# Kernel optimization log

Measured on AMD Instinct MI355X. Metric: run time of the kernel, lower is better.

## Reference

```python
import jax, jax.numpy as jnp
import numpy as np

RSQRT2 = 2 ** (-0.5)
B, S, D_IN = 2, 4096, 1024
H, D_HEAD = 8, 64            # num_heads, attention_dim (per-head qk and v dim)
QK_DIM = H * D_HEAD          # 512
V_DIM = H * D_HEAD           # 512
OUT_DIM = D_IN               # 1024 (output_dim defaults to input_dim)
LN_EPS = 1e-5


def setup_inputs() -> dict:
    key = jax.random.key(0)
    ks = jax.random.split(key, 8)
    def lecun(k, fan_in, shape):
        return jax.random.normal(k, shape, dtype=jnp.float32) * (1.0 / np.sqrt(fan_in))
    return {
        "x": jax.random.normal(ks[0], (B, S, D_IN), dtype=jnp.float32),
        # weights stored [in, out] (transposed torch Linear layout)
        "W_qk": lecun(ks[1], D_IN, (D_IN, 2 * QK_DIM)),
        "b_qk": jnp.zeros((2 * QK_DIM,), jnp.float32),
        "W_v": lecun(ks[2], D_IN, (D_IN, V_DIM)),
        "b_v": jnp.zeros((V_DIM,), jnp.float32),
        "W_out": lecun(ks[3], V_DIM, (V_DIM, OUT_DIM)),
        "b_out": jnp.zeros((OUT_DIM,), jnp.float32),
        "ln_gamma": jnp.ones((OUT_DIM,), jnp.float32),
        "ln_beta": jnp.zeros((OUT_DIM,), jnp.float32),
    }


def _layernorm(y, gamma, beta):
    mu = jnp.mean(y, axis=-1, keepdims=True)
    var = jnp.mean(jnp.square(y - mu), axis=-1, keepdims=True)
    return (y - mu) * jax.lax.rsqrt(var + LN_EPS) * gamma + beta


def reference(x, W_qk, b_qk, W_v, b_v, W_out, b_out, ln_gamma, ln_beta):
    b, s, _ = x.shape
    scale = D_HEAD ** (-0.5)
    qk = x @ W_qk + b_qk                          # [b, s, 2*h*d]
    qk = qk.reshape(b, s, H, D_HEAD, 2)           # c (q/k) is fastest axis
    q, k = qk[..., 0], qk[..., 1]                 # [b, s, h, d]
    v = (x @ W_v + b_v).reshape(b, s, H, D_HEAD)  # [b, s, h, d]
    # manual multi-head attention, full O(s^2) score matrix (as in source)
    sim = jnp.einsum("bihd,bjhd->bhij", q, k) * scale
    attn = jax.nn.softmax(sim, axis=-1)           # [b, h, i, j]
    o = jnp.einsum("bhij,bjhd->bihd", attn, v)    # [b, s, h, d]
    o = o.reshape(b, s, V_DIM)                    # 'b h s d -> b s (h d)'
    y = _layernorm(o @ W_out + b_out, ln_gamma, ln_beta)
    return (y + x) * RSQRT2
```

## Files before the change

kernel.cpp:

```cpp
#include <hip/hip_runtime.h>
#include <stdint.h>

typedef short bf16x8 __attribute__((ext_vector_type(8)));
typedef float f32x4 __attribute__((ext_vector_type(4)));
typedef unsigned short ushort_t;

#define RSQRT2_F 0.70710678118654752440f
#define QSCALE_F 0.18033688011114382f

__device__ __forceinline__ ushort_t f2bf(float f) {
  union { float f; uint32_t u; } c; c.f = f;
  uint32_t u = c.u;
  uint32_t r = (u + 0x7fffu + ((u >> 16) & 1u)) >> 16;
  return (ushort_t)r;
}
__device__ __forceinline__ float bf2f(ushort_t u) {
  union { uint32_t u; float f; } c; c.u = ((uint32_t)u) << 16;
  return c.f;
}
__device__ __forceinline__ uint32_t fbits(float f) {
  union { float f; uint32_t u; } c; c.f = f; return c.u;
}

__device__ __forceinline__ void gload_lds16(const void* g, void* l) {
  __builtin_amdgcn_global_load_lds(
      (const __attribute__((address_space(1))) void*)g,
      (__attribute__((address_space(3))) void*)l, 16, 0, 0);
}

__global__ __launch_bounds__(256) void k_cvt_x(const float* __restrict__ x,
                                               ushort_t* __restrict__ xb) {
  int i = (blockIdx.x * 256 + threadIdx.x) * 4;
  float4 f = *(const float4*)(x + i);
  ushort4 o;
  o.x = f2bf(f.x); o.y = f2bf(f.y); o.z = f2bf(f.z); o.w = f2bf(f.w);
  *(ushort4*)(xb + i) = o;
}

__global__ __launch_bounds__(256) void k_build_wqkv(const float* __restrict__ Wqk,
                                                    const float* __restrict__ bqk,
                                                    const float* __restrict__ Wv,
                                                    const float* __restrict__ bv,
                                                    ushort_t* __restrict__ Wt,
                                                    float* __restrict__ biasAll) {
  int k = blockIdx.x * 256 + threadIdx.x;
  int n = blockIdx.y;
  float w, bb;
  if (n < 512)       { w = Wqk[(size_t)k * 1024 + 2 * n] * QSCALE_F;     bb = bqk[2 * n] * QSCALE_F; }
  else if (n < 1024) { w = Wqk[(size_t)k * 1024 + 2 * (n - 512) + 1];    bb = bqk[2 * (n - 512) + 1]; }
  else               { w = Wv[(size_t)k * 512 + (n - 1024)];             bb = bv[n - 1024]; }
  Wt[(size_t)n * 1024 + k] = f2bf(w);
  if (k == 0) biasAll[n] = bb;
}

__global__ __launch_bounds__(256) void k_build_wout(const float* __restrict__ Wout,
                                                    ushort_t* __restrict__ Wt) {
  int k = blockIdx.x * 256 + threadIdx.x;
  int n = blockIdx.y;
  Wt[(size_t)n * 512 + k] = f2bf(Wout[(size_t)k * 1024 + n]);
}

template <int MODE>
__global__ __launch_bounds__(256) void k_gemm_bt(
    const ushort_t* __restrict__ A, const ushort_t* __restrict__ Bt,
    const float* __restrict__ bias,
    ushort_t* __restrict__ out0, ushort_t* __restrict__ out1, ushort_t* __restrict__ out2,
    int M, int N, int K) {
  __shared__ __align__(16) ushort_t As[2][4][128][8];
  __shared__ __align__(16) ushort_t Bs[2][4][128][8];
  const int t = threadIdx.x;
  const int lane = t & 63;
  const int wave = t >> 6;

  const int nby = N >> 7;
  const int nwg = gridDim.x;
  const int xcd = blockIdx.x & 7, pos = blockIdx.x >> 3;
  const int swz = xcd * (nwg >> 3) + pos;
  const int bx = swz / nby, by = swz % nby;
  const int m0 = bx * 128, n0 = by * 128;

  const int wm = (wave >> 1) * 64, wn = (wave & 1) * 64;
  const int lg = lane >> 4, lr = lane & 15;

  const int srow = t & 127, sg = t >> 7;
  const ushort_t* gA = A + (size_t)(m0 + srow) * K + sg * 8;
  const ushort_t* gB = Bt + (size_t)(n0 + srow) * K + sg * 8;

  f32x4 acc[4][4] = {};

#define GEMM_STAGE(k0, bsel)                                   \
  do {                                                         \
    gload_lds16(gA + (k0), &As[bsel][sg][srow][0]);            \
    gload_lds16(gA + (k0) + 16, &As[bsel][sg + 2][srow][0]);   \
    gload_lds16(gB + (k0), &Bs[bsel][sg][srow][0]);            \
    gload_lds16(gB + (k0) + 16, &Bs[bsel][sg + 2][srow][0]);   \
  } while (0)

  GEMM_STAGE(0, 0);
  __syncthreads();
  int buf = 0;
  for (int k0 = 0; k0 < K; k0 += 32) {
    if (k0 + 32 < K) GEMM_STAGE(k0 + 32, buf ^ 1);
    bf16x8 af[4], bfr[4];
#pragma unroll
    for (int mi = 0; mi < 4; mi++) af[mi] = *(const bf16x8*)&As[buf][lg][wm + mi * 16 + lr][0];
#pragma unroll
    for (int ni = 0; ni < 4; ni++) bfr[ni] = *(const bf16x8*)&Bs[buf][lg][wn + ni * 16 + lr][0];
#pragma unroll
    for (int mi = 0; mi < 4; mi++)
#pragma unroll
      for (int ni = 0; ni < 4; ni++)
        acc[mi][ni] = __builtin_amdgcn_mfma_f32_16x16x32_bf16(af[mi], bfr[ni], acc[mi][ni], 0, 0, 0);
    __syncthreads();
    buf ^= 1;
  }
#undef GEMM_STAGE

#pragma unroll
  for (int mi = 0; mi < 4; mi++) {
    int rowb = m0 + wm + mi * 16 + (lane >> 4) * 4;
#pragma unroll
    for (int ni = 0; ni < 4; ni++) {
      int col = n0 + wn + ni * 16 + lr;
      float bc = bias[col];
#pragma unroll
      for (int reg = 0; reg < 4; reg++) {
        int row = rowb + reg;
        float v = acc[mi][ni][reg] + bc;
        if (MODE == 0) {
          if (col < 512) {
            out0[(size_t)row * 512 + col] = f2bf(v);
          } else if (col < 1024) {
            out1[(size_t)row * 512 + (col - 512)] = f2bf(v);
          } else {
            int hd = col - 1024;
            int bb = row >> 12, s = row & 4095;
            out2[((size_t)(bb << 9) + hd) * 4096 + s] = f2bf(v);
          }
        } else {
          out0[(size_t)row * 1024 + col] = f2bf(v);
        }
      }
    }
  }
}

__global__ __launch_bounds__(256, 2) void k_attn(const ushort_t* __restrict__ Qb,
                                                 const ushort_t* __restrict__ Kb,
                                                 const ushort_t* __restrict__ Vt,
                                                 ushort_t* __restrict__ O0,
                                                 ushort_t* __restrict__ O1,
                                                 ushort_t* __restrict__ O2,
                                                 ushort_t* __restrict__ O3,
                                                 float* __restrict__ lpart) {
  __shared__ __align__(16) ushort_t Ks[2][8][64][8];
  __shared__ __align__(16) ushort_t Vs[2][8][64][8];
  __shared__ __align__(16) ushort_t Pl[4][1024];
  const int S = 4096;
  const int t = threadIdx.x, lane = t & 63, wave = t >> 6;
  const int lg = lane >> 4, lr = lane & 15;

  const int bid = blockIdx.x;
  const int xcd = bid & 7, idx = bid >> 3;
  const int bh = (xcd << 1) | (idx >> 6);
  const int rem = idx & 63;
  const int qb = rem >> 2;
  const int quarter = rem & 3;
  const int b = bh >> 3, h = bh & 7;
  const int qbase = qb * 256 + wave * 64;
  const int kvbase = quarter * 1024;

  bf16x8 qf[4][2];
#pragma unroll
  for (int su = 0; su < 4; su++) {
    const ushort_t* qp = Qb + ((size_t)(b * S + qbase + su * 16 + lr)) * 512 + h * 64 + lg * 8;
    qf[su][0] = *(const bf16x8*)qp;
    qf[su][1] = *(const bf16x8*)(qp + 32);
  }

  const int cj = t & 63, cg = t >> 6;
  const ushort_t* gK = Kb + ((size_t)b * S + cj) * 512 + h * 64 + cg * 8;
  const ushort_t* gV = Vt + ((size_t)bh * 64 + cj) * 4096 + cg * 8;

  const bf16x8 vones = {(short)0x3F80, (short)0x3F80, (short)0x3F80, (short)0x3F80,
                        (short)0x3F80, (short)0x3F80, (short)0x3F80, (short)0x3F80};

  int poff[4], pread[2];
#pragma unroll
  for (int nt = 0; nt < 4; nt++) poff[nt] = (lr * 128 + nt * 32 + lg * 8) ^ ((lr & 7) << 4);
#pragma unroll
  for (int kc = 0; kc < 2; kc++) pread[kc] = (lr * 128 + kc * 64 + lg * 16) ^ ((lr & 7) << 4);

  f32x4 of[4][4] = {};
  f32x4 of_sum[4] = {};

#define ATTN_STAGE(kv0, bsel)                                         \
  do {                                                                \
    gload_lds16(gK + (size_t)(kv0) * 512, &Ks[bsel][cg][cj][0]);      \
    gload_lds16(gK + (size_t)(kv0) * 512 + 32, &Ks[bsel][cg + 4][cj][0]); \
    gload_lds16(gV + (kv0), &Vs[bsel][cg][cj][0]);                    \
    gload_lds16(gV + (kv0) + 32, &Vs[bsel][cg + 4][cj][0]);           \
  } while (0)

  ATTN_STAGE(kvbase, 0);
  __syncthreads();
  int buf = 0;

  for (int kv0 = kvbase; kv0 < kvbase + 1024; kv0 += 64) {
    if (kv0 + 64 < kvbase + 1024) ATTN_STAGE(kv0 + 64, buf ^ 1);

    f32x4 sf[4][4];
    __builtin_amdgcn_s_setprio(1);
#pragma unroll
    for (int nt = 0; nt < 4; nt++) {
      bf16x8 kf0 = *(const bf16x8*)&Ks[buf][lg][nt * 16 + lr][0];
      bf16x8 kf1 = *(const bf16x8*)&Ks[buf][4 + lg][nt * 16 + lr][0];
#pragma unroll
      for (int su = 0; su < 4; su++) {
        f32x4 z = {};
        z = __builtin_amdgcn_mfma_f32_16x16x32_bf16(kf0, qf[su][0], z, 0, 0, 0);
        sf[su][nt] = __builtin_amdgcn_mfma_f32_16x16x32_bf16(kf1, qf[su][1], z, 0, 0, 0);
      }
    }
    __builtin_amdgcn_s_setprio(0);

    bf16x8 pf[4][2];
#pragma unroll
    for (int su = 0; su < 4; su++) {
      char* Pb = (char*)&Pl[wave][0];
#pragma unroll
      for (int nt = 0; nt < 4; nt++) {
        float p0 = __builtin_amdgcn_exp2f(sf[su][nt][0]);
        float p1 = __builtin_amdgcn_exp2f(sf[su][nt][1]);
        float p2 = __builtin_amdgcn_exp2f(sf[su][nt][2]);
        float p3 = __builtin_amdgcn_exp2f(sf[su][nt][3]);
        uint32_t w0 = (fbits(p0) >> 16) | (fbits(p1) & 0xffff0000u);
        uint32_t w1 = (fbits(p2) >> 16) | (fbits(p3) & 0xffff0000u);
        *(uint2*)(Pb + poff[nt]) = make_uint2(w0, w1);
      }
#pragma unroll
      for (int kc = 0; kc < 2; kc++) pf[su][kc] = *(const bf16x8*)(Pb + pread[kc]);
    }

    __builtin_amdgcn_s_setprio(1);
#pragma unroll
    for (int dt = 0; dt < 4; dt++) {
      bf16x8 vf0 = *(const bf16x8*)&Vs[buf][lg][dt * 16 + lr][0];
      bf16x8 vf1 = *(const bf16x8*)&Vs[buf][4 + lg][dt * 16 + lr][0];
#pragma unroll
      for (int su = 0; su < 4; su++) {
        of[su][dt] = __builtin_amdgcn_mfma_f32_16x16x32_bf16(pf[su][0], vf0, of[su][dt], 0, 0, 0);
        of[su][dt] = __builtin_amdgcn_mfma_f32_16x16x32_bf16(pf[su][1], vf1, of[su][dt], 0, 0, 0);
      }
    }
#pragma unroll
    for (int su = 0; su < 4; su++) {
      of_sum[su] = __builtin_amdgcn_mfma_f32_16x16x32_bf16(pf[su][0], vones, of_sum[su], 0, 0, 0);
      of_sum[su] = __builtin_amdgcn_mfma_f32_16x16x32_bf16(pf[su][1], vones, of_sum[su], 0, 0, 0);
    }
    __builtin_amdgcn_s_setprio(0);

    __syncthreads();
    buf ^= 1;
  }
#undef ATTN_STAGE

  ushort_t* Opq = (quarter == 0) ? O0 : (quarter == 1) ? O1 : (quarter == 2) ? O2 : O3;
  ushort_t* Opw = Opq + (size_t)b * 4096 * 512;
#pragma unroll
  for (int su = 0; su < 4; su++) {
#pragma unroll
    for (int dt = 0; dt < 4; dt++)
#pragma unroll
      for (int r = 0; r < 4; r++) {
        int q = qbase + su * 16 + lg * 4 + r;
        Opw[(size_t)q * 512 + h * 64 + dt * 16 + lr] = f2bf(of[su][dt][r]);
      }
    if (lr == 0) {
#pragma unroll
      for (int r = 0; r < 4; r++) {
        int q = qbase + su * 16 + lg * 4 + r;
        lpart[(((size_t)quarter * 2 + b) * 8 + h) * 4096 + q] = of_sum[su][r];
      }
    }
  }
}

__global__ __launch_bounds__(128) void k_merge(const ushort_t* __restrict__ O0,
                                               const ushort_t* __restrict__ O1,
                                               const ushort_t* __restrict__ O2,
                                               const ushort_t* __restrict__ O3,
                                               const float* __restrict__ lpart,
                                               ushort_t* __restrict__ Ob) {
  const int row = blockIdx.x;
  const int t = threadIdx.x;
  const int col = t * 4;
  const int b = row >> 12, q = row & 4095;
  const int h = col >> 6;
  float l = 0.f;
#pragma unroll
  for (int qu = 0; qu < 4; qu++)
    l += lpart[(((size_t)qu * 2 + b) * 8 + h) * 4096 + q];
  float inv = 1.0f / l;
  ushort4 a0 = *(const ushort4*)(O0 + (size_t)row * 512 + col);
  ushort4 a1 = *(const ushort4*)(O1 + (size_t)row * 512 + col);
  ushort4 a2 = *(const ushort4*)(O2 + (size_t)row * 512 + col);
  ushort4 a3 = *(const ushort4*)(O3 + (size_t)row * 512 + col);
  ushort4 o;
  o.x = f2bf((bf2f(a0.x) + bf2f(a1.x) + bf2f(a2.x) + bf2f(a3.x)) * inv);
  o.y = f2bf((bf2f(a0.y) + bf2f(a1.y) + bf2f(a2.y) + bf2f(a3.y)) * inv);
  o.z = f2bf((bf2f(a0.z) + bf2f(a1.z) + bf2f(a2.z) + bf2f(a3.z)) * inv);
  o.w = f2bf((bf2f(a0.w) + bf2f(a1.w) + bf2f(a2.w) + bf2f(a3.w)) * inv);
  *(ushort4*)(Ob + (size_t)row * 512 + col) = o;
}

__global__ __launch_bounds__(256) void k_ln(const ushort_t* __restrict__ ypre,
                                            const float* __restrict__ x,
                                            const float* __restrict__ gamma,
                                            const float* __restrict__ beta,
                                            float* __restrict__ out) {
  __shared__ float red[8];
  const int row = blockIdx.x, t = threadIdx.x;
  const ushort_t* yr = ypre + (size_t)row * 1024;
  ushort4 u = *(const ushort4*)(yr + t * 4);
  float v0 = bf2f(u.x), v1 = bf2f(u.y), v2 = bf2f(u.z), v3 = bf2f(u.w);
  float s = v0 + v1 + v2 + v3;
  float sq = v0 * v0 + v1 * v1 + v2 * v2 + v3 * v3;
#pragma unroll
  for (int m = 32; m; m >>= 1) { s += __shfl_xor(s, m, 64); sq += __shfl_xor(sq, m, 64); }
  if ((t & 63) == 0) { red[t >> 6] = s; red[4 + (t >> 6)] = sq; }
  __syncthreads();
  s = red[0] + red[1] + red[2] + red[3];
  sq = red[4] + red[5] + red[6] + red[7];
  float mu = s * (1.f / 1024.f);
  float var = sq * (1.f / 1024.f) - mu * mu;
  float inv = rsqrtf(var + 1e-5f);
  int c = t * 4;
  float4 xf = *(const float4*)(x + (size_t)row * 1024 + c);
  float4 o;
  o.x = ((v0 - mu) * inv * gamma[c + 0] + beta[c + 0] + xf.x) * RSQRT2_F;
  o.y = ((v1 - mu) * inv * gamma[c + 1] + beta[c + 1] + xf.y) * RSQRT2_F;
  o.z = ((v2 - mu) * inv * gamma[c + 2] + beta[c + 2] + xf.z) * RSQRT2_F;
  o.w = ((v3 - mu) * inv * gamma[c + 3] + beta[c + 3] + xf.w) * RSQRT2_F;
  *(float4*)(out + (size_t)row * 1024 + c) = o;
}

extern "C" void kernel_launch(void* const* d_in, const int* in_sizes, int n_in,
                              void* d_out, int out_size, void* d_ws, size_t ws_size,
                              hipStream_t stream) {
  (void)in_sizes; (void)n_in; (void)out_size; (void)ws_size;
  const float* x     = (const float*)d_in[0];
  const float* Wqk   = (const float*)d_in[1];
  const float* bqk   = (const float*)d_in[2];
  const float* Wv    = (const float*)d_in[3];
  const float* bv    = (const float*)d_in[4];
  const float* Wout  = (const float*)d_in[5];
  const float* bout  = (const float*)d_in[6];
  const float* gamma = (const float*)d_in[7];
  const float* beta  = (const float*)d_in[8];
  float* out = (float*)d_out;

  char* ws = (char*)d_ws;
  size_t off = 0;
  auto alloc = [&](size_t bytes) {
    off = (off + 255) & ~(size_t)255;
    void* p = ws + off;
    off += bytes;
    return p;
  };
  ushort_t* xb    = (ushort_t*)alloc(8192ull * 1024 * 2);
  ushort_t* Wqkvt = (ushort_t*)alloc(1536ull * 1024 * 2);
  float*    biasA = (float*)   alloc(1536ull * 4);
  ushort_t* Woutt = (ushort_t*)alloc(1024ull * 512 * 2);
  ushort_t* Qb    = (ushort_t*)alloc(8192ull * 512 * 2);
  ushort_t* Kbuf  = (ushort_t*)alloc(8192ull * 512 * 2);
  ushort_t* Vtb   = (ushort_t*)alloc(1024ull * 4096 * 2);
  ushort_t* Oq2   = (ushort_t*)alloc(8192ull * 512 * 2);
  ushort_t* Oq3   = (ushort_t*)alloc(8192ull * 512 * 2);
  float*    lpart = (float*)   alloc(4ull * 2 * 8 * 4096 * 4);
  ushort_t* Oq0   = xb;
  ushort_t* Oq1   = xb + 8192ull * 512;
  ushort_t* Obm   = Qb;
  ushort_t* ypre  = xb;

  k_cvt_x<<<8192, 256, 0, stream>>>(x, xb);
  k_build_wqkv<<<dim3(4, 1536), 256, 0, stream>>>(Wqk, bqk, Wv, bv, Wqkvt, biasA);
  k_build_wout<<<dim3(2, 1024), 256, 0, stream>>>(Wout, Woutt);
  k_gemm_bt<0><<<768, 256, 0, stream>>>(xb, Wqkvt, biasA, Qb, Kbuf, Vtb, 8192, 1536, 1024);
  k_attn<<<1024, 256, 0, stream>>>(Qb, Kbuf, Vtb, Oq0, Oq1, Oq2, Oq3, lpart);
  k_merge<<<8192, 128, 0, stream>>>(Oq0, Oq1, Oq2, Oq3, lpart, Obm);
  k_gemm_bt<1><<<512, 256, 0, stream>>>(Obm, Woutt, bout, ypre, nullptr, nullptr, 8192, 1024, 512);
  k_ln<<<8192, 256, 0, stream>>>(ypre, x, gamma, beta, out);
}
```

Baseline: 207.4 us.

## Halve attention query tile, single-buffer GEMM LDS, and regroup GEMM tile order

The attention kernel now assigns 32 query rows per wave (128 per block) instead of 64, doubling the grid to 2048 blocks and halving accumulator registers. The GEMM drops LDS double-buffering in favour of a single buffer with two barriers per k-step. It also replaces the XCD-aware swizzle with a 2D grid that groups 4 M-tiles per N column for L2 reuse. Smaller attention tiles cost K/V reuse per block but may raise occupancy. Removing the prefetch exposes global load latency in the GEMM.

Result: slower. 211.6 us (+2.0%).

```diff
diff --git a/kernel.cpp b/kernel.cpp
--- a/kernel.cpp
+++ b/kernel.cpp
@@ -66,55 +66,50 @@
     const float* __restrict__ bias,
     ushort_t* __restrict__ out0, ushort_t* __restrict__ out1, ushort_t* __restrict__ out2,
     int M, int N, int K) {
-  __shared__ __align__(16) ushort_t As[2][4][128][8];
-  __shared__ __align__(16) ushort_t Bs[2][4][128][8];
+  __shared__ __align__(16) ushort_t As[4][128][8];
+  __shared__ __align__(16) ushort_t Bs[4][128][8];
   const int t = threadIdx.x;
   const int lane = t & 63;
   const int wave = t >> 6;
 
-  const int nby = N >> 7;
-  const int nwg = gridDim.x;
-  const int xcd = blockIdx.x & 7, pos = blockIdx.x >> 3;
-  const int swz = xcd * (nwg >> 3) + pos;
-  const int bx = swz / nby, by = swz % nby;
-  const int m0 = bx * 128, n0 = by * 128;
+  const int id = blockIdx.y * gridDim.x + blockIdx.x;
+  const int nby = gridDim.y;
+  const int per = 4 * nby;
+  const int sid = id / per, w = id % per;
+  const int mt = sid * 4 + (w & 3), nt = w >> 2;
+  const int m0 = mt * 128, n0 = nt * 128;
 
   const int wm = (wave >> 1) * 64, wn = (wave & 1) * 64;
   const int lg = lane >> 4, lr = lane & 15;
 
   const int srow = t & 127, sg = t >> 7;
+  ushort_t* lA0 = &As[sg][srow][0];
+  ushort_t* lA1 = &As[sg + 2][srow][0];
+  ushort_t* lB0 = &Bs[sg][srow][0];
+  ushort_t* lB1 = &Bs[sg + 2][srow][0];
   const ushort_t* gA = A + (size_t)(m0 + srow) * K + sg * 8;
   const ushort_t* gB = Bt + (size_t)(n0 + srow) * K + sg * 8;
 
   f32x4 acc[4][4] = {};
 
-#define GEMM_STAGE(k0, bsel)                                   \
-  do {                                                         \
-    gload_lds16(gA + (k0), &As[bsel][sg][srow][0]);            \
-    gload_lds16(gA + (k0) + 16, &As[bsel][sg + 2][srow][0]);   \
-    gload_lds16(gB + (k0), &Bs[bsel][sg][srow][0]);            \
-    gload_lds16(gB + (k0) + 16, &Bs[bsel][sg + 2][srow][0]);   \
-  } while (0)
-
-  GEMM_STAGE(0, 0);
-  __syncthreads();
-  int buf = 0;
   for (int k0 = 0; k0 < K; k0 += 32) {
-    if (k0 + 32 < K) GEMM_STAGE(k0 + 32, buf ^ 1);
+    __syncthreads();
+    gload_lds16(gA + k0, lA0);
+    gload_lds16(gA + k0 + 16, lA1);
+    gload_lds16(gB + k0, lB0);
+    gload_lds16(gB + k0 + 16, lB1);
+    __syncthreads();
     bf16x8 af[4], bfr[4];
 #pragma unroll
-    for (int mi = 0; mi < 4; mi++) af[mi] = *(const bf16x8*)&As[buf][lg][wm + mi * 16 + lr][0];
-#pragma unroll
-    for (int ni = 0; ni < 4; ni++) bfr[ni] = *(const bf16x8*)&Bs[buf][lg][wn + ni * 16 + lr][0];
+    for (int mi = 0; mi < 4; mi++) af[mi] = *(const bf16x8*)&As[lg][wm + mi * 16 + lr][0];
+#pragma unroll
+    for (int ni = 0; ni < 4; ni++) bfr[ni] = *(const bf16x8*)&Bs[lg][wn + ni * 16 + lr][0];
 #pragma unroll
     for (int mi = 0; mi < 4; mi++)
 #pragma unroll
       for (int ni = 0; ni < 4; ni++)
         acc[mi][ni] = __builtin_amdgcn_mfma_f32_16x16x32_bf16(af[mi], bfr[ni], acc[mi][ni], 0, 0, 0);
-    __syncthreads();
-    buf ^= 1;
-  }
-#undef GEMM_STAGE
+  }
 
 #pragma unroll
   for (int mi = 0; mi < 4; mi++) {
@@ -162,17 +157,17 @@
 
   const int bid = blockIdx.x;
   const int xcd = bid & 7, idx = bid >> 3;
-  const int bh = (xcd << 1) | (idx >> 6);
-  const int rem = idx & 63;
+  const int bh = (xcd << 1) | (idx >> 7);
+  const int rem = idx & 127;
   const int qb = rem >> 2;
   const int quarter = rem & 3;
   const int b = bh >> 3, h = bh & 7;
-  const int qbase = qb * 256 + wave * 64;
+  const int qbase = qb * 128 + wave * 32;
   const int kvbase = quarter * 1024;
 
-  bf16x8 qf[4][2];
-#pragma unroll
-  for (int su = 0; su < 4; su++) {
+  bf16x8 qf[2][2];
+#pragma unroll
+  for (int su = 0; su < 2; su++) {
     const ushort_t* qp = Qb + ((size_t)(b * S + qbase + su * 16 + lr)) * 512 + h * 64 + lg * 8;
     qf[su][0] = *(const bf16x8*)qp;
     qf[su][1] = *(const bf16x8*)(qp + 32);
@@ -191,8 +186,8 @@
 #pragma unroll
   for (int kc = 0; kc < 2; kc++) pread[kc] = (lr * 128 + kc * 64 + lg * 16) ^ ((lr & 7) << 4);
 
-  f32x4 of[4][4] = {};
-  f32x4 of_sum[4] = {};
+  f32x4 of[2][4] = {};
+  f32x4 of_sum[2] = {};
 
 #define ATTN_STAGE(kv0, bsel)                                         \
   do {                                                                \
@@ -209,14 +204,14 @@
   for (int kv0 = kvbase; kv0 < kvbase + 1024; kv0 += 64) {
     if (kv0 + 64 < kvbase + 1024) ATTN_STAGE(kv0 + 64, buf ^ 1);
 
-    f32x4 sf[4][4];
+    f32x4 sf[2][4];
     __builtin_amdgcn_s_setprio(1);
 #pragma unroll
     for (int nt = 0; nt < 4; nt++) {
       bf16x8 kf0 = *(const bf16x8*)&Ks[buf][lg][nt * 16 + lr][0];
       bf16x8 kf1 = *(const bf16x8*)&Ks[buf][4 + lg][nt * 16 + lr][0];
 #pragma unroll
-      for (int su = 0; su < 4; su++) {
+      for (int su = 0; su < 2; su++) {
         f32x4 z = {};
         z = __builtin_amdgcn_mfma_f32_16x16x32_bf16(kf0, qf[su][0], z, 0, 0, 0);
         sf[su][nt] = __builtin_amdgcn_mfma_f32_16x16x32_bf16(kf1, qf[su][1], z, 0, 0, 0);
@@ -224,9 +219,9 @@
     }
     __builtin_amdgcn_s_setprio(0);
 
-    bf16x8 pf[4][2];
-#pragma unroll
-    for (int su = 0; su < 4; su++) {
+    bf16x8 pf[2][2];
+#pragma unroll
+    for (int su = 0; su < 2; su++) {
       char* Pb = (char*)&Pl[wave][0];
 #pragma unroll
       for (int nt = 0; nt < 4; nt++) {
@@ -248,13 +243,13 @@
       bf16x8 vf0 = *(const bf16x8*)&Vs[buf][lg][dt * 16 + lr][0];
       bf16x8 vf1 = *(const bf16x8*)&Vs[buf][4 + lg][dt * 16 + lr][0];
 #pragma unroll
-      for (int su = 0; su < 4; su++) {
+      for (int su = 0; su < 2; su++) {
         of[su][dt] = __builtin_amdgcn_mfma_f32_16x16x32_bf16(pf[su][0], vf0, of[su][dt], 0, 0, 0);
         of[su][dt] = __builtin_amdgcn_mfma_f32_16x16x32_bf16(pf[su][1], vf1, of[su][dt], 0, 0, 0);
       }
     }
 #pragma unroll
-    for (int su = 0; su < 4; su++) {
+    for (int su = 0; su < 2; su++) {
       of_sum[su] = __builtin_amdgcn_mfma_f32_16x16x32_bf16(pf[su][0], vones, of_sum[su], 0, 0, 0);
       of_sum[su] = __builtin_amdgcn_mfma_f32_16x16x32_bf16(pf[su][1], vones, of_sum[su], 0, 0, 0);
     }
@@ -268,7 +263,7 @@
   ushort_t* Opq = (quarter == 0) ? O0 : (quarter == 1) ? O1 : (quarter == 2) ? O2 : O3;
   ushort_t* Opw = Opq + (size_t)b * 4096 * 512;
 #pragma unroll
-  for (int su = 0; su < 4; su++) {
+  for (int su = 0; su < 2; su++) {
 #pragma unroll
     for (int dt = 0; dt < 4; dt++)
 #pragma unroll
@@ -386,9 +381,9 @@
   k_cvt_x<<<8192, 256, 0, stream>>>(x, xb);
   k_build_wqkv<<<dim3(4, 1536), 256, 0, stream>>>(Wqk, bqk, Wv, bv, Wqkvt, biasA);
   k_build_wout<<<dim3(2, 1024), 256, 0, stream>>>(Wout, Woutt);
-  k_gemm_bt<0><<<768, 256, 0, stream>>>(xb, Wqkvt, biasA, Qb, Kbuf, Vtb, 8192, 1536, 1024);
-  k_attn<<<1024, 256, 0, stream>>>(Qb, Kbuf, Vtb, Oq0, Oq1, Oq2, Oq3, lpart);
+  k_gemm_bt<0><<<dim3(64, 12), 256, 0, stream>>>(xb, Wqkvt, biasA, Qb, Kbuf, Vtb, 8192, 1536, 1024);
+  k_attn<<<2048, 256, 0, stream>>>(Qb, Kbuf, Vtb, Oq0, Oq1, Oq2, Oq3, lpart);
   k_merge<<<8192, 128, 0, stream>>>(Oq0, Oq1, Oq2, Oq3, lpart, Obm);
-  k_gemm_bt<1><<<512, 256, 0, stream>>>(Obm, Woutt, bout, ypre, nullptr, nullptr, 8192, 1024, 512);
+  k_gemm_bt<1><<<dim3(64, 8), 256, 0, stream>>>(Obm, Woutt, bout, ypre, nullptr, nullptr, 8192, 1024, 512);
   k_ln<<<8192, 256, 0, stream>>>(ypre, x, gamma, beta, out);
 }
```
